# Kernel optimization log

Measured on AMD Instinct MI355X. Metric: run time of the kernel, lower is better.

The kernel has to match this reference:

```python
import jax, jax.numpy as jnp
import numpy as np

B, C, H, I, O = 256, 128, 1024, 512, 128

def setup_inputs() -> dict:
    key = jax.random.key(0)
    k1, k2, k3, k4, k5 = jax.random.split(key, 5)
    return {
        "x": jax.random.normal(k1, (B, C, 1, I), dtype=jnp.float32),
        "w1": jax.random.normal(k2, (C, H, I), dtype=jnp.float32) * 0.05,
        "b1": jax.random.normal(k3, (1, C, H), dtype=jnp.float32) * 0.05,
        "w2": jax.random.normal(k4, (C, O, H), dtype=jnp.float32) * 0.05,
        "b2": jax.random.normal(k5, (1, C, O), dtype=jnp.float32) * 0.05,
    }

def reference(x, w1, b1, w2, b2):
    # x: (B, C, 1, I). Per-channel linear 1: (x*w1).sum(-1)+b1 == einsum over I.
    xs = x[:, :, 0, :]                                   # (B, C, I)
    h = jax.nn.relu(jnp.einsum('bci,chi->bch', xs, w1) + b1)  # (B, C, H)
    # Per-channel linear 2: (h.unsqueeze(2)*w2).sum(-1)+b2
    logit = jnp.einsum('bch,coh->bco', h, w2) + b2       # (B, C, O)
    return jnp.swapaxes(logit, 1, 2)                     # (B, O, C)
```

## Files before the change

kernel.cpp:

```cpp
#include <hip/hip_runtime.h>

#define Bdim 256
#define Cdim 128
#define Hdim 1024
#define Idim 512
#define Odim 128

#define BT 64
#define HT 128
#define BK 64

#define XS_LD  72
#define W1S_LD 72
#define W2S_LD 136
#define HS_LD  136

typedef __attribute__((ext_vector_type(8))) short short8;
typedef __attribute__((ext_vector_type(4))) float f32x4;

__global__ __launch_bounds__(256, 2) void mlp_fused(
    const float* __restrict__ x, const float* __restrict__ w1,
    const float* __restrict__ b1, const float* __restrict__ w2,
    const float* __restrict__ b2, float* __restrict__ out)
{
    __shared__ unsigned char smem[52224];
    unsigned short* Xs  = (unsigned short*)smem;
    unsigned short* W1s = (unsigned short*)(smem + 9216);
    unsigned short* W2s = (unsigned short*)smem;
    unsigned short* Hs  = (unsigned short*)(smem + 34816);

    const int t    = threadIdx.x;
    const int lane = t & 63;
    const int q    = lane >> 4;
    const int r16  = lane & 15;
    const int wave = t >> 6;
    const int wm   = wave >> 1;
    const int wn   = wave & 1;

    const int bid = blockIdx.x;
    const int g   = bid & 7;
    const int s   = bid >> 3;
    const int c   = g * 16 + (s & 15);
    const int bt  = s >> 4;
    const int row0 = bt * BT;

    const int tx    = t & 15;
    const int trow  = t >> 4;
    const int tx32  = t & 31;
    const int trow8 = t >> 5;

    const float* xbase  = x  + ((size_t)row0 * Cdim + c) * Idim;
    const float* w1base = w1 + (size_t)c * Hdim * Idim;
    const float* w2base = w2 + (size_t)c * Odim * Hdim;

    f32x4 acc2[2][4];
    for (int j = 0; j < 4; ++j) {
        float bv = b2[c * Odim + wn * 64 + j * 16 + r16];
        f32x4 z = {bv, bv, bv, bv};
        acc2[0][j] = z;
        acc2[1][j] = z;
    }

    for (int ht = 0; ht < Hdim / HT; ++ht) {
        f32x4 acc1[2][4];
        {
            f32x4 z = {0.f, 0.f, 0.f, 0.f};
            for (int i = 0; i < 2; ++i)
                for (int j = 0; j < 4; ++j) acc1[i][j] = z;
        }

        for (int kt = 0; kt < Idim / BK; ++kt) {
            __syncthreads();
            #pragma unroll
            for (int p = 0; p < 8; ++p) {
                int rr = trow + p * 16;
                float4 v = *(const float4*)(w1base + (size_t)(ht * HT + rr) * Idim + kt * BK + tx * 4);
                unsigned int lo = __builtin_amdgcn_perm(__float_as_uint(v.y), __float_as_uint(v.x), 0x07060302);
                unsigned int hi = __builtin_amdgcn_perm(__float_as_uint(v.w), __float_as_uint(v.z), 0x07060302);
                *(uint2*)&W1s[rr * W1S_LD + tx * 4] = make_uint2(lo, hi);
                if (p < 4) {
                    float4 xv = *(const float4*)(xbase + (size_t)rr * (Cdim * Idim) + kt * BK + tx * 4);
                    unsigned int xlo = __builtin_amdgcn_perm(__float_as_uint(xv.y), __float_as_uint(xv.x), 0x07060302);
                    unsigned int xhi = __builtin_amdgcn_perm(__float_as_uint(xv.w), __float_as_uint(xv.z), 0x07060302);
                    *(uint2*)&Xs[rr * XS_LD + tx * 4] = make_uint2(xlo, xhi);
                }
            }
            __syncthreads();
            #pragma unroll
            for (int ks = 0; ks < 2; ++ks) {
                int k0 = ks * 32 + q * 8;
                short8 a[2], b[4];
                #pragma unroll
                for (int i = 0; i < 2; ++i)
                    a[i] = *(const short8*)&Xs[(wm * 32 + i * 16 + r16) * XS_LD + k0];
                #pragma unroll
                for (int j = 0; j < 4; ++j)
                    b[j] = *(const short8*)&W1s[(wn * 64 + j * 16 + r16) * W1S_LD + k0];
                #pragma unroll
                for (int i = 0; i < 2; ++i)
                    #pragma unroll
                    for (int j = 0; j < 4; ++j)
                        acc1[i][j] = __builtin_amdgcn_mfma_f32_16x16x32_bf16(a[i], b[j], acc1[i][j], 0, 0, 0);
            }
        }
        __syncthreads();

        #pragma unroll
        for (int p = 0; p < 16; ++p) {
            int rr = trow8 + p * 8;
            float4 v = *(const float4*)(w2base + (size_t)rr * Hdim + ht * HT + tx32 * 4);
            unsigned int lo = __builtin_amdgcn_perm(__float_as_uint(v.y), __float_as_uint(v.x), 0x07060302);
            unsigned int hi = __builtin_amdgcn_perm(__float_as_uint(v.w), __float_as_uint(v.z), 0x07060302);
            *(uint2*)&W2s[rr * W2S_LD + tx32 * 4] = make_uint2(lo, hi);
        }
        for (int j = 0; j < 4; ++j) {
            int n = wn * 64 + j * 16 + r16;
            float b1v = b1[c * Hdim + ht * HT + n];
            #pragma unroll
            for (int i = 0; i < 2; ++i) {
                #pragma unroll
                for (int r = 0; r < 4; ++r) {
                    int m = wm * 32 + i * 16 + q * 4 + r;
                    float hv = fmaxf(acc1[i][j][r] + b1v, 0.f);
                    Hs[m * HS_LD + n] = (unsigned short)(__float_as_uint(hv) >> 16);
                }
            }
        }
        __syncthreads();
        #pragma unroll
        for (int ks = 0; ks < 4; ++ks) {
            int k0 = ks * 32 + q * 8;
            short8 a[2], b[4];
            #pragma unroll
            for (int i = 0; i < 2; ++i)
                a[i] = *(const short8*)&Hs[(wm * 32 + i * 16 + r16) * HS_LD + k0];
            #pragma unroll
            for (int j = 0; j < 4; ++j)
                b[j] = *(const short8*)&W2s[(wn * 64 + j * 16 + r16) * W2S_LD + k0];
            #pragma unroll
            for (int i = 0; i < 2; ++i)
                #pragma unroll
                for (int j = 0; j < 4; ++j)
                    acc2[i][j] = __builtin_amdgcn_mfma_f32_16x16x32_bf16(a[i], b[j], acc2[i][j], 0, 0, 0);
        }
    }

    #pragma unroll
    for (int i = 0; i < 2; ++i)
        #pragma unroll
        for (int j = 0; j < 4; ++j)
            #pragma unroll
            for (int r = 0; r < 4; ++r) {
                int bb = row0 + wm * 32 + i * 16 + q * 4 + r;
                int o  = wn * 64 + j * 16 + r16;
                out[(size_t)bb * (Odim * Cdim) + o * Cdim + c] = acc2[i][j][r];
            }
}

extern "C" void kernel_launch(void* const* d_in, const int* in_sizes, int n_in,
                              void* d_out, int out_size, void* d_ws, size_t ws_size,
                              hipStream_t stream) {
    const float* x  = (const float*)d_in[0];
    const float* w1 = (const float*)d_in[1];
    const float* b1 = (const float*)d_in[2];
    const float* w2 = (const float*)d_in[3];
    const float* b2 = (const float*)d_in[4];
    float* out = (float*)d_out;
    mlp_fused<<<dim3(512), dim3(256), 0, stream>>>(x, w1, b1, w2, b2, out);
}
```

Before: 527.3 us.

## Load MFMA operands directly from global memory, bypassing LDS staging for X, W1, W2

Drops the shared-memory staging of X, W1 and W2 tiles. Each lane now loads its own fp32 operand fragments straight from global memory and converts them to bf16 in registers before the MFMA. This removes the LDS writes and reads and the two barriers per K step of the first GEMM, and shrinks LDS to the hidden-activation buffer only. In exchange, operands shared between waves are fetched redundantly from global/L2 (W1 rows by both wm waves, X rows by both wn waves), and each lane reads 32 contiguous bytes per row rather than loads coalesced across lanes.

```diff
diff --git a/kernel.cpp b/kernel.cpp
--- a/kernel.cpp
+++ b/kernel.cpp
@@ -8,26 +8,26 @@
 
 #define BT 64
 #define HT 128
-#define BK 64
-
-#define XS_LD  72
-#define W1S_LD 72
-#define W2S_LD 136
-#define HS_LD  136
+#define HS_LD 136
 
 typedef __attribute__((ext_vector_type(8))) short short8;
 typedef __attribute__((ext_vector_type(4))) float f32x4;
+
+__device__ __forceinline__ short8 cvt8(float4 v0, float4 v1) {
+    union { unsigned int u[4]; short8 s; } r;
+    r.u[0] = __builtin_amdgcn_perm(__float_as_uint(v0.y), __float_as_uint(v0.x), 0x07060302);
+    r.u[1] = __builtin_amdgcn_perm(__float_as_uint(v0.w), __float_as_uint(v0.z), 0x07060302);
+    r.u[2] = __builtin_amdgcn_perm(__float_as_uint(v1.y), __float_as_uint(v1.x), 0x07060302);
+    r.u[3] = __builtin_amdgcn_perm(__float_as_uint(v1.w), __float_as_uint(v1.z), 0x07060302);
+    return r.s;
+}
 
 __global__ __launch_bounds__(256, 2) void mlp_fused(
     const float* __restrict__ x, const float* __restrict__ w1,
     const float* __restrict__ b1, const float* __restrict__ w2,
     const float* __restrict__ b2, float* __restrict__ out)
 {
-    __shared__ unsigned char smem[52224];
-    unsigned short* Xs  = (unsigned short*)smem;
-    unsigned short* W1s = (unsigned short*)(smem + 9216);
-    unsigned short* W2s = (unsigned short*)smem;
-    unsigned short* Hs  = (unsigned short*)(smem + 34816);
+    __shared__ unsigned short Hs[BT * HS_LD];
 
     const int t    = threadIdx.x;
     const int lane = t & 63;
@@ -44,16 +44,16 @@
     const int bt  = s >> 4;
     const int row0 = bt * BT;
 
-    const int tx    = t & 15;
-    const int trow  = t >> 4;
-    const int tx32  = t & 31;
-    const int trow8 = t >> 5;
-
-    const float* xbase  = x  + ((size_t)row0 * Cdim + c) * Idim;
-    const float* w1base = w1 + (size_t)c * Hdim * Idim;
-    const float* w2base = w2 + (size_t)c * Odim * Hdim;
+    const float* xr0 = x + ((size_t)(row0 + wm * 32 + r16) * Cdim + c) * Idim;
+    const float* xr1 = xr0 + (size_t)16 * Cdim * Idim;
+    const float* w1c = w1 + (size_t)c * Hdim * Idim;
+    const float* w2r[4];
+    #pragma unroll
+    for (int j = 0; j < 4; ++j)
+        w2r[j] = w2 + ((size_t)c * Odim + wn * 64 + j * 16 + r16) * Hdim;
 
     f32x4 acc2[2][4];
+    #pragma unroll
     for (int j = 0; j < 4; ++j) {
         float bv = b2[c * Odim + wn * 64 + j * 16 + r16];
         f32x4 z = {bv, bv, bv, bv};
@@ -63,80 +63,60 @@
 
     for (int ht = 0; ht < Hdim / HT; ++ht) {
         f32x4 acc1[2][4];
-        {
-            f32x4 z = {0.f, 0.f, 0.f, 0.f};
+        #pragma unroll
+        for (int i = 0; i < 2; ++i)
+            #pragma unroll
+            for (int j = 0; j < 4; ++j) acc1[i][j] = (f32x4){0.f, 0.f, 0.f, 0.f};
+
+        const float* w1r0 = w1c + (size_t)(ht * HT + wn * 64 + r16) * Idim;
+
+        #pragma unroll 2
+        for (int ks = 0; ks < Idim / 32; ++ks) {
+            const int k0 = ks * 32 + q * 8;
+            short8 a[2], b[4];
+            a[0] = cvt8(*(const float4*)(xr0 + k0), *(const float4*)(xr0 + k0 + 4));
+            a[1] = cvt8(*(const float4*)(xr1 + k0), *(const float4*)(xr1 + k0 + 4));
+            #pragma unroll
+            for (int j = 0; j < 4; ++j) {
+                const float* p = w1r0 + (size_t)(j * 16) * Idim + k0;
+                b[j] = cvt8(*(const float4*)p, *(const float4*)(p + 4));
+            }
+            #pragma unroll
             for (int i = 0; i < 2; ++i)
-                for (int j = 0; j < 4; ++j) acc1[i][j] = z;
+                #pragma unroll
+                for (int j = 0; j < 4; ++j)
+                    acc1[i][j] = __builtin_amdgcn_mfma_f32_16x16x32_bf16(a[i], b[j], acc1[i][j], 0, 0, 0);
         }
 
-        for (int kt = 0; kt < Idim / BK; ++kt) {
-            __syncthreads();
+        __syncthreads();
+        #pragma unroll
+        for (int j = 0; j < 4; ++j) {
+            const int n = wn * 64 + j * 16 + r16;
+            const float b1v = b1[c * Hdim + ht * HT + n];
             #pragma unroll
-            for (int p = 0; p < 8; ++p) {
-                int rr = trow + p * 16;
-                float4 v = *(const float4*)(w1base + (size_t)(ht * HT + rr) * Idim + kt * BK + tx * 4);
-                unsigned int lo = __builtin_amdgcn_perm(__float_as_uint(v.y), __float_as_uint(v.x), 0x07060302);
-                unsigned int hi = __builtin_amdgcn_perm(__float_as_uint(v.w), __float_as_uint(v.z), 0x07060302);
-                *(uint2*)&W1s[rr * W1S_LD + tx * 4] = make_uint2(lo, hi);
-                if (p < 4) {
-                    float4 xv = *(const float4*)(xbase + (size_t)rr * (Cdim * Idim) + kt * BK + tx * 4);
-                    unsigned int xlo = __builtin_amdgcn_perm(__float_as_uint(xv.y), __float_as_uint(xv.x), 0x07060302);
-                    unsigned int xhi = __builtin_amdgcn_perm(__float_as_uint(xv.w), __float_as_uint(xv.z), 0x07060302);
-                    *(uint2*)&Xs[rr * XS_LD + tx * 4] = make_uint2(xlo, xhi);
+            for (int i = 0; i < 2; ++i) {
+                #pragma unroll
+                for (int r = 0; r < 4; ++r) {
+                    const int m = wm * 32 + i * 16 + q * 4 + r;
+                    const float hv = fmaxf(acc1[i][j][r] + b1v, 0.f);
+                    Hs[m * HS_LD + n] = (unsigned short)(__float_as_uint(hv) >> 16);
                 }
-            }
-            __syncthreads();
-            #pragma unroll
-            for (int ks = 0; ks < 2; ++ks) {
-                int k0 = ks * 32 + q * 8;
-                short8 a[2], b[4];
-                #pragma unroll
-                for (int i = 0; i < 2; ++i)
-                    a[i] = *(const short8*)&Xs[(wm * 32 + i * 16 + r16) * XS_LD + k0];
-                #pragma unroll
-                for (int j = 0; j < 4; ++j)
-                    b[j] = *(const short8*)&W1s[(wn * 64 + j * 16 + r16) * W1S_LD + k0];
-                #pragma unroll
-                for (int i = 0; i < 2; ++i)
-                    #pragma unroll
-                    for (int j = 0; j < 4; ++j)
-                        acc1[i][j] = __builtin_amdgcn_mfma_f32_16x16x32_bf16(a[i], b[j], acc1[i][j], 0, 0, 0);
             }
         }
         __syncthreads();
 
         #pragma unroll
-        for (int p = 0; p < 16; ++p) {
-            int rr = trow8 + p * 8;
-            float4 v = *(const float4*)(w2base + (size_t)rr * Hdim + ht * HT + tx32 * 4);
-            unsigned int lo = __builtin_amdgcn_perm(__float_as_uint(v.y), __float_as_uint(v.x), 0x07060302);
-            unsigned int hi = __builtin_amdgcn_perm(__float_as_uint(v.w), __float_as_uint(v.z), 0x07060302);
-            *(uint2*)&W2s[rr * W2S_LD + tx32 * 4] = make_uint2(lo, hi);
-        }
-        for (int j = 0; j < 4; ++j) {
-            int n = wn * 64 + j * 16 + r16;
-            float b1v = b1[c * Hdim + ht * HT + n];
-            #pragma unroll
-            for (int i = 0; i < 2; ++i) {
-                #pragma unroll
-                for (int r = 0; r < 4; ++r) {
-                    int m = wm * 32 + i * 16 + q * 4 + r;
-                    float hv = fmaxf(acc1[i][j][r] + b1v, 0.f);
-                    Hs[m * HS_LD + n] = (unsigned short)(__float_as_uint(hv) >> 16);
-                }
-            }
-        }
-        __syncthreads();
-        #pragma unroll
-        for (int ks = 0; ks < 4; ++ks) {
-            int k0 = ks * 32 + q * 8;
+        for (int ks = 0; ks < HT / 32; ++ks) {
+            const int k0 = ks * 32 + q * 8;
             short8 a[2], b[4];
             #pragma unroll
             for (int i = 0; i < 2; ++i)
                 a[i] = *(const short8*)&Hs[(wm * 32 + i * 16 + r16) * HS_LD + k0];
             #pragma unroll
-            for (int j = 0; j < 4; ++j)
-                b[j] = *(const short8*)&W2s[(wn * 64 + j * 16 + r16) * W2S_LD + k0];
+            for (int j = 0; j < 4; ++j) {
+                const float* p = w2r[j] + ht * HT + k0;
+                b[j] = cvt8(*(const float4*)p, *(const float4*)(p + 4));
+            }
             #pragma unroll
             for (int i = 0; i < 2; ++i)
                 #pragma unroll
@@ -151,8 +131,8 @@
         for (int j = 0; j < 4; ++j)
             #pragma unroll
             for (int r = 0; r < 4; ++r) {
-                int bb = row0 + wm * 32 + i * 16 + q * 4 + r;
-                int o  = wn * 64 + j * 16 + r16;
+                const int bb = row0 + wm * 32 + i * 16 + q * 4 + r;
+                const int o  = wn * 64 + j * 16 + r16;
                 out[(size_t)bb * (Odim * Cdim) + o * Cdim + c] = acc2[i][j][r];
             }
 }
```

Result: slower. 837.2 us (+58.8%).

## Register-prefetch next global tiles and replace syncthreads with raw barriers

Applied to the files above, without the earlier changes.

Global loads for the next W1/X k-tile, and for the W2 slice on the last k-step, are issued into registers before the MFMA loop so their latency overlaps compute. Full __syncthreads are replaced with s_barrier plus an explicit lgkmcnt(0) wait, so outstanding global loads no longer drain at each barrier. This adds many float4 registers (pw, px, qw), which risks spills or lower occupancy under launch_bounds(256,2).

```diff
diff --git a/kernel.cpp b/kernel.cpp
--- a/kernel.cpp
+++ b/kernel.cpp
@@ -17,6 +17,16 @@
 
 typedef __attribute__((ext_vector_type(8))) short short8;
 typedef __attribute__((ext_vector_type(4))) float f32x4;
+
+#define FENCE()  asm volatile("" ::: "memory")
+#define BAR()    __builtin_amdgcn_s_barrier()
+#define LGKM0()  asm volatile("s_waitcnt lgkmcnt(0)" ::: "memory")
+
+__device__ __forceinline__ uint2 cvt4(float4 v) {
+    unsigned int lo = __builtin_amdgcn_perm(__float_as_uint(v.y), __float_as_uint(v.x), 0x07060302);
+    unsigned int hi = __builtin_amdgcn_perm(__float_as_uint(v.w), __float_as_uint(v.z), 0x07060302);
+    return make_uint2(lo, hi);
+}
 
 __global__ __launch_bounds__(256, 2) void mlp_fused(
     const float* __restrict__ x, const float* __restrict__ w1,
@@ -54,6 +64,7 @@
     const float* w2base = w2 + (size_t)c * Odim * Hdim;
 
     f32x4 acc2[2][4];
+    #pragma unroll
     for (int j = 0; j < 4; ++j) {
         float bv = b2[c * Odim + wn * 64 + j * 16 + r16];
         f32x4 z = {bv, bv, bv, bv};
@@ -61,31 +72,45 @@
         acc2[1][j] = z;
     }
 
+    float4 pw[8], px[4], qw[16];
+
+    #pragma unroll
+    for (int p = 0; p < 8; ++p)
+        pw[p] = *(const float4*)(w1base + (size_t)(trow + p * 16) * Idim + tx * 4);
+    #pragma unroll
+    for (int p = 0; p < 4; ++p)
+        px[p] = *(const float4*)(xbase + (size_t)(trow + p * 16) * (Cdim * Idim) + tx * 4);
+
     for (int ht = 0; ht < Hdim / HT; ++ht) {
         f32x4 acc1[2][4];
-        {
-            f32x4 z = {0.f, 0.f, 0.f, 0.f};
-            for (int i = 0; i < 2; ++i)
-                for (int j = 0; j < 4; ++j) acc1[i][j] = z;
-        }
+        #pragma unroll
+        for (int i = 0; i < 2; ++i)
+            #pragma unroll
+            for (int j = 0; j < 4; ++j) acc1[i][j] = (f32x4){0.f, 0.f, 0.f, 0.f};
 
         for (int kt = 0; kt < Idim / BK; ++kt) {
-            __syncthreads();
-            #pragma unroll
-            for (int p = 0; p < 8; ++p) {
-                int rr = trow + p * 16;
-                float4 v = *(const float4*)(w1base + (size_t)(ht * HT + rr) * Idim + kt * BK + tx * 4);
-                unsigned int lo = __builtin_amdgcn_perm(__float_as_uint(v.y), __float_as_uint(v.x), 0x07060302);
-                unsigned int hi = __builtin_amdgcn_perm(__float_as_uint(v.w), __float_as_uint(v.z), 0x07060302);
-                *(uint2*)&W1s[rr * W1S_LD + tx * 4] = make_uint2(lo, hi);
-                if (p < 4) {
-                    float4 xv = *(const float4*)(xbase + (size_t)rr * (Cdim * Idim) + kt * BK + tx * 4);
-                    unsigned int xlo = __builtin_amdgcn_perm(__float_as_uint(xv.y), __float_as_uint(xv.x), 0x07060302);
-                    unsigned int xhi = __builtin_amdgcn_perm(__float_as_uint(xv.w), __float_as_uint(xv.z), 0x07060302);
-                    *(uint2*)&Xs[rr * XS_LD + tx * 4] = make_uint2(xlo, xhi);
-                }
-            }
-            __syncthreads();
+            FENCE();
+            BAR();
+            #pragma unroll
+            for (int p = 0; p < 8; ++p)
+                *(uint2*)&W1s[(trow + p * 16) * W1S_LD + tx * 4] = cvt4(pw[p]);
+            #pragma unroll
+            for (int p = 0; p < 4; ++p)
+                *(uint2*)&Xs[(trow + p * 16) * XS_LD + tx * 4] = cvt4(px[p]);
+            if (kt < Idim / BK - 1) {
+                #pragma unroll
+                for (int p = 0; p < 8; ++p)
+                    pw[p] = *(const float4*)(w1base + (size_t)(ht * HT + trow + p * 16) * Idim + (kt + 1) * BK + tx * 4);
+                #pragma unroll
+                for (int p = 0; p < 4; ++p)
+                    px[p] = *(const float4*)(xbase + (size_t)(trow + p * 16) * (Cdim * Idim) + (kt + 1) * BK + tx * 4);
+            } else {
+                #pragma unroll
+                for (int p = 0; p < 16; ++p)
+                    qw[p] = *(const float4*)(w2base + (size_t)(trow8 + p * 8) * Hdim + ht * HT + tx32 * 4);
+            }
+            LGKM0();
+            BAR();
             #pragma unroll
             for (int ks = 0; ks < 2; ++ks) {
                 int k0 = ks * 32 + q * 8;
@@ -103,16 +128,15 @@
                         acc1[i][j] = __builtin_amdgcn_mfma_f32_16x16x32_bf16(a[i], b[j], acc1[i][j], 0, 0, 0);
             }
         }
-        __syncthreads();
-
-        #pragma unroll
-        for (int p = 0; p < 16; ++p) {
-            int rr = trow8 + p * 8;
-            float4 v = *(const float4*)(w2base + (size_t)rr * Hdim + ht * HT + tx32 * 4);
-            unsigned int lo = __builtin_amdgcn_perm(__float_as_uint(v.y), __float_as_uint(v.x), 0x07060302);
-            unsigned int hi = __builtin_amdgcn_perm(__float_as_uint(v.w), __float_as_uint(v.z), 0x07060302);
-            *(uint2*)&W2s[rr * W2S_LD + tx32 * 4] = make_uint2(lo, hi);
-        }
+
+        FENCE();
+        BAR();
+
+        #pragma unroll
+        for (int p = 0; p < 16; ++p)
+            *(uint2*)&W2s[(trow8 + p * 8) * W2S_LD + tx32 * 4] = cvt4(qw[p]);
+
+        #pragma unroll
         for (int j = 0; j < 4; ++j) {
             int n = wn * 64 + j * 16 + r16;
             float b1v = b1[c * Hdim + ht * HT + n];
@@ -126,7 +150,19 @@
                 }
             }
         }
-        __syncthreads();
+
+        if (ht < Hdim / HT - 1) {
+            #pragma unroll
+            for (int p = 0; p < 8; ++p)
+                pw[p] = *(const float4*)(w1base + (size_t)((ht + 1) * HT + trow + p * 16) * Idim + tx * 4);
+            #pragma unroll
+            for (int p = 0; p < 4; ++p)
+                px[p] = *(const float4*)(xbase + (size_t)(trow + p * 16) * (Cdim * Idim) + tx * 4);
+        }
+
+        LGKM0();
+        BAR();
+
         #pragma unroll
         for (int ks = 0; ks < 4; ++ks) {
             int k0 = ks * 32 + q * 8;
```

Result: no change. 519.0 us (-1.6%).
